# Kernel optimization log

Hardware: AMD Instinct MI355X
Metric: run time of the kernel (lower is better)

Reference implementation:

```python
import jax, jax.numpy as jnp
import numpy as np

NUM_HEADS = 8
SCALE_BASE = 512.0
GN_EPS = 1e-5


def rotate_every_two(x):
    x1 = x[..., ::2]
    x2 = x[..., 1::2]
    return jnp.stack([-x2, x1], axis=-1).reshape(x.shape)


def xpos_apply(x, downscale):
    # x: [B, T, D]; XPOS rotary with length-dependent scale (offset=0)
    L, D = x.shape[1], x.shape[2]
    half = D // 2
    scale_vec = (jnp.arange(0, D, 2, dtype=jnp.float32) + 0.4 * D) / (1.4 * D)  # [half]
    pos = jnp.arange(L, dtype=jnp.float32)
    scale = scale_vec[None, :] ** (pos[:, None] / SCALE_BASE)  # [L, half]
    inv_freq = 1.0 / (10000.0 ** (jnp.arange(half, dtype=jnp.float32) / half))
    sinusoid = pos[:, None] * inv_freq[None, :]  # [L, half]
    sin, cos = jnp.sin(sinusoid), jnp.cos(sinusoid)
    if downscale:
        scale = 1.0 / scale
    sin_s = jnp.repeat(sin * scale, 2, axis=-1)  # duplicate_interleave -> [L, D]
    cos_s = jnp.repeat(cos * scale, 2, axis=-1)
    return x * cos_s + rotate_every_two(x) * sin_s


def decay_mask_fn(T, num_heads):
    # gamma per head; decay stored as log(gamma) so mask = gamma^(i-j) on lower triangle
    s, e = np.log(1.0 / 32.0), np.log(1.0 / 512.0)
    gamma = 1.0 - jnp.exp(jnp.linspace(s, e, num_heads).astype(jnp.float32))
    log_decay = jnp.log(gamma)  # [H], negative
    idx = jnp.arange(T)
    expo = (idx[:, None] - idx[None, :]).astype(jnp.float32)  # i - j
    tri = (idx[:, None] >= idx[None, :])
    expo_safe = jnp.where(tri, expo, 0.0)
    mask = jnp.exp(log_decay[:, None, None] * expo_safe) * tri  # [H, T, T]
    scale = jnp.sqrt(mask.sum(axis=-1, keepdims=True))  # [H, T, 1]
    return mask / scale


def setup_inputs() -> dict:
    key = jax.random.key(0)
    ks = jax.random.split(key, 4)
    B, T, E = 2, 2048, 1024
    V = 2 * E
    return {
        "hidden_states": jax.random.normal(ks[0], (B, T, E), dtype=jnp.float32),
        "w_qkv": jax.random.normal(ks[1], (E, 2 * E + V), dtype=jnp.float32) * 0.02,
        "b_qkv": jnp.zeros((2 * E + V,), dtype=jnp.float32),
        "w_g": jax.random.normal(ks[2], (E, V), dtype=jnp.float32) * 0.02,
        "b_g": jnp.zeros((V,), dtype=jnp.float32),
        "w_p": jax.random.normal(ks[3], (V, E), dtype=jnp.float32) * 0.02,
        "b_p": jnp.zeros((E,), dtype=jnp.float32),
    }


def reference(hidden_states, w_qkv, b_qkv, w_g, b_g, w_p, b_p):
    B, T, E = hidden_states.shape
    H = NUM_HEADS
    V = 2 * E
    dk, dv = E // H, V // H

    qkv = hidden_states @ w_qkv + b_qkv
    q, k, v = qkv[..., :E], qkv[..., E:2 * E], qkv[..., 2 * E:]
    q = xpos_apply(q, downscale=False)
    k = xpos_apply(k, downscale=True)

    # split heads -> [B, H, T, d]
    q = q.reshape(B, T, H, dk).transpose(0, 2, 1, 3)
    k = k.reshape(B, T, H, dk).transpose(0, 2, 1, 3)
    v = v.reshape(B, T, H, dv).transpose(0, 2, 1, 3)

    mask = decay_mask_fn(T, H)  # [H, T, T]

    # parallel retention
    retention = jnp.einsum("bhid,bhjd->bhij", q, k) * (dk ** -0.5)
    retention = retention * mask[None]  # [B, H, T, T]
    out = jnp.einsum("bhij,bhjv->bhiv", retention, v)

    # current_kv = sum_j mask[h, -1, j] * k_j (x) v_j
    curr_kv = jnp.einsum("hj,bhjk,bhjv->bhkv", mask[:, -1, :], k, v)

    retention_out = out.transpose(0, 2, 1, 3).reshape(B, T, V)

    # GroupNorm(num_groups=H, affine=False) over v_dim channels
    g = retention_out.reshape(B * T, H, dv)
    mu = g.mean(axis=-1, keepdims=True)
    var = ((g - mu) ** 2).mean(axis=-1, keepdims=True)
    normed = ((g - mu) / jnp.sqrt(var + GN_EPS)).reshape(B, T, V)

    gated = jax.nn.silu(hidden_states @ w_g + b_g) * normed
    proj = gated @ w_p + b_p
    return proj, curr_kv
```

## Files before the change

kernel.cpp:

```cpp
#include <hip/hip_runtime.h>
#include <math.h>

#define BT      4096
#define T_SEQ   2048
#define E_DIM   1024
#define V_DIM   2048
#define DK      128
#define DV      256
#define QKV_LD  4096

typedef unsigned short ushort_t;
typedef __attribute__((ext_vector_type(8)))  short bf16x8;
typedef __attribute__((ext_vector_type(4)))  unsigned short u16x4;
typedef __attribute__((ext_vector_type(16))) float f32x16;

__device__ __forceinline__ void decay_params(int h, float& ld, float& gamma) {
    const float s0 = -3.4657359027997265f;
    const float e0 = -6.2383246250395092f;
    float lin = s0 + (e0 - s0) * ((float)h * (1.0f / 7.0f));
    gamma = 1.0f - expf(lin);
    ld = logf(gamma);
}

__device__ __forceinline__ short f2bf(float f) {
    unsigned u = __float_as_uint(f);
    unsigned r = (u + 0x7fffu + ((u >> 16) & 1u)) >> 16;
    return (short)r;
}
__device__ __forceinline__ float bf2f(ushort_t u) {
    return __uint_as_float((unsigned)u << 16);
}

__device__ __forceinline__ void async_copy16(void* lds, const void* g) {
    __builtin_amdgcn_global_load_lds(
        (const __attribute__((address_space(1))) unsigned int*)g,
        (__attribute__((address_space(3))) unsigned int*)lds, 16, 0, 0);
}

__global__ __launch_bounds__(256)
void f32_to_bf16_kernel(const float* __restrict__ in, ushort_t* __restrict__ out)
{
    int i = (blockIdx.x * 256 + threadIdx.x) * 8;
    float4 a = *(const float4*)&in[i];
    float4 b = *(const float4*)&in[i + 4];
    bf16x8 o;
    o[0] = f2bf(a.x); o[1] = f2bf(a.y); o[2] = f2bf(a.z); o[3] = f2bf(a.w);
    o[4] = f2bf(b.x); o[5] = f2bf(b.y); o[6] = f2bf(b.z); o[7] = f2bf(b.w);
    *(bf16x8*)&out[i] = o;
}

__global__ __launch_bounds__(256)
void transpose_w_kernel(const float* __restrict__ W, ushort_t* __restrict__ Wt,
                        int K, int N)
{
    __shared__ float tile[32][33];
    const int k0 = blockIdx.y * 32, n0 = blockIdx.x * 32;
    const int t = threadIdx.x;
    const int r = t >> 3, c = (t & 7) * 4;
    float4 v = *(const float4*)&W[(size_t)(k0 + r) * N + n0 + c];
    tile[r][c] = v.x; tile[r][c + 1] = v.y; tile[r][c + 2] = v.z; tile[r][c + 3] = v.w;
    __syncthreads();
    u16x4 o;
    o[0] = (ushort_t)f2bf(tile[c][r]);
    o[1] = (ushort_t)f2bf(tile[c + 1][r]);
    o[2] = (ushort_t)f2bf(tile[c + 2][r]);
    o[3] = (ushort_t)f2bf(tile[c + 3][r]);
    *(u16x4*)&Wt[(size_t)(n0 + r) * K + k0 + c] = o;
}

template<int EPI>
__global__ __launch_bounds__(256)
void gemm_bf16(const ushort_t* __restrict__ A, int lda,
               const ushort_t* __restrict__ Bt, int ldb,
               const float* __restrict__ bias,
               void* __restrict__ Cv, int ldc,
               const void* __restrict__ extra, int lde,
               int nkt)
{
    __shared__ ushort_t As[2 * 128 * 32];
    __shared__ ushort_t Bs[2 * 128 * 32];

    const int tid = threadIdx.x;
    const int w  = tid >> 6, l = tid & 63;
    const int lc = l & 31, q = l >> 5;
    const int wr = w >> 1, wc = w & 1;
    const int m0 = blockIdx.y * 128, n0 = blockIdx.x * 128;

    const int r0 = tid >> 2,         kc0 = (tid & 3) ^ ((r0 >> 1) & 3);
    const int r1 = (256 + tid) >> 2, kc1 = (tid & 3) ^ ((r1 >> 1) & 3);
    const ushort_t* gA0 = A  + (size_t)(m0 + r0) * lda + kc0 * 8;
    const ushort_t* gA1 = A  + (size_t)(m0 + r1) * lda + kc1 * 8;
    const ushort_t* gB0 = Bt + (size_t)(n0 + r0) * ldb + kc0 * 8;
    const ushort_t* gB1 = Bt + (size_t)(n0 + r1) * ldb + kc1 * 8;
    const int s0 = w * 512;
    const int s1 = 2048 + w * 512;

    const int sl = (lc >> 1) & 3;
    int aoff[2][2], boff[2][2];
    #pragma unroll
    for (int mi = 0; mi < 2; ++mi)
        #pragma unroll
        for (int ks = 0; ks < 2; ++ks) {
            const int kc = ks * 2 + q;
            aoff[mi][ks] = ((wr * 64 + mi * 32 + lc) * 4 + (kc ^ sl)) * 8;
            boff[mi][ks] = ((wc * 64 + mi * 32 + lc) * 4 + (kc ^ sl)) * 8;
        }

    f32x16 acc[2][2];
    #pragma unroll
    for (int mi = 0; mi < 2; ++mi)
        #pragma unroll
        for (int ni = 0; ni < 2; ++ni)
            #pragma unroll
            for (int e = 0; e < 16; ++e) acc[mi][ni][e] = 0.0f;

    auto stage = [&](int bb) {
        async_copy16(&As[bb + s0], gA0); async_copy16(&As[bb + s1], gA1);
        async_copy16(&Bs[bb + s0], gB0); async_copy16(&Bs[bb + s1], gB1);
        gA0 += 32; gA1 += 32; gB0 += 32; gB1 += 32;
    };
    auto compute = [&](int cb) {
        bf16x8 a[2][2], b[2][2];
        #pragma unroll
        for (int mi = 0; mi < 2; ++mi)
            #pragma unroll
            for (int ks = 0; ks < 2; ++ks) {
                a[mi][ks] = *(const bf16x8*)&As[cb + aoff[mi][ks]];
                b[mi][ks] = *(const bf16x8*)&Bs[cb + boff[mi][ks]];
            }
        #pragma unroll
        for (int ks = 0; ks < 2; ++ks)
            #pragma unroll
            for (int mi = 0; mi < 2; ++mi)
                #pragma unroll
                for (int ni = 0; ni < 2; ++ni)
                    acc[mi][ni] = __builtin_amdgcn_mfma_f32_32x32x16_bf16(
                        a[mi][ks], b[ni][ks], acc[mi][ni], 0, 0, 0);
    };

    stage(0);
    __syncthreads();
    for (int kt = 0; kt < nkt - 2; kt += 2) {
        stage(4096); compute(0);    __syncthreads();
        stage(0);    compute(4096); __syncthreads();
    }
    stage(4096); compute(0); __syncthreads();
    compute(4096);

    #pragma unroll
    for (int ni = 0; ni < 2; ++ni) {
        const int col = n0 + wc * 64 + ni * 32 + lc;
        const float bb = bias[col];
        #pragma unroll
        for (int mi = 0; mi < 2; ++mi) {
            #pragma unroll
            for (int r = 0; r < 16; ++r) {
                const int row = m0 + wr * 64 + mi * 32 + (r & 3) + 8 * (r >> 2) + 4 * q;
                float val = acc[mi][ni][r] + bb;
                if (EPI == 0) {
                    ((float*)Cv)[(size_t)row * ldc + col] = val;
                } else {
                    const float e = bf2f(((const ushort_t*)extra)[(size_t)row * lde + col]);
                    val = val / (1.0f + expf(-val)) * e;
                    ((ushort_t*)Cv)[(size_t)row * ldc + col] = (ushort_t)f2bf(val);
                }
            }
        }
    }
}

__global__ __launch_bounds__(256)
void gemm_tm64(const ushort_t* __restrict__ A, int lda,
               const ushort_t* __restrict__ Bt, int ldb,
               const float* __restrict__ bias,
               float* __restrict__ C, int ldc, int nkt)
{
    __shared__ ushort_t As[2 * 64 * 32];
    __shared__ ushort_t Bs[2 * 128 * 32];

    const int tid = threadIdx.x;
    const int w  = tid >> 6, l = tid & 63;
    const int lc = l & 31, q = l >> 5;
    const int wr = w >> 1, wc = w & 1;
    const int m0 = blockIdx.y * 64, n0 = blockIdx.x * 128;

    const int rA = tid >> 2,          kcA = (tid & 3) ^ ((rA >> 1) & 3);
    const int rB1 = (256 + tid) >> 2, kcB1 = (tid & 3) ^ ((rB1 >> 1) & 3);
    const ushort_t* gA  = A  + (size_t)(m0 + rA)  * lda + kcA  * 8;
    const ushort_t* gB0 = Bt + (size_t)(n0 + rA)  * ldb + kcA  * 8;
    const ushort_t* gB1 = Bt + (size_t)(n0 + rB1) * ldb + kcB1 * 8;
    const int sA  = w * 512;
    const int sB0 = w * 512;
    const int sB1 = 2048 + w * 512;

    const int sl = (lc >> 1) & 3;
    int aoff[2], boff[2][2];
    #pragma unroll
    for (int ks = 0; ks < 2; ++ks) {
        const int kc = ks * 2 + q;
        const int mrow = wr * 32 + lc;
        aoff[ks] = (mrow * 4 + (kc ^ sl)) * 8;
        #pragma unroll
        for (int ni = 0; ni < 2; ++ni) {
            const int nrow = wc * 64 + ni * 32 + lc;
            boff[ni][ks] = (nrow * 4 + (kc ^ sl)) * 8;
        }
    }

    f32x16 acc[2];
    #pragma unroll
    for (int ni = 0; ni < 2; ++ni)
        #pragma unroll
        for (int e = 0; e < 16; ++e) acc[ni][e] = 0.0f;

    auto stage = [&](int ab, int bb) {
        async_copy16(&As[ab + sA], gA);
        async_copy16(&Bs[bb + sB0], gB0); async_copy16(&Bs[bb + sB1], gB1);
        gA += 32; gB0 += 32; gB1 += 32;
    };
    auto compute = [&](int ab, int bb) {
        bf16x8 a[2], b[2][2];
        #pragma unroll
        for (int ks = 0; ks < 2; ++ks) {
            a[ks] = *(const bf16x8*)&As[ab + aoff[ks]];
            b[0][ks] = *(const bf16x8*)&Bs[bb + boff[0][ks]];
            b[1][ks] = *(const bf16x8*)&Bs[bb + boff[1][ks]];
        }
        #pragma unroll
        for (int ks = 0; ks < 2; ++ks)
            #pragma unroll
            for (int ni = 0; ni < 2; ++ni)
                acc[ni] = __builtin_amdgcn_mfma_f32_32x32x16_bf16(
                    a[ks], b[ni][ks], acc[ni], 0, 0, 0);
    };

    stage(0, 0);
    __syncthreads();
    for (int kt = 0; kt < nkt - 2; kt += 2) {
        stage(2048, 4096); compute(0, 0);       __syncthreads();
        stage(0, 0);       compute(2048, 4096); __syncthreads();
    }
    stage(2048, 4096); compute(0, 0); __syncthreads();
    compute(2048, 4096);

    #pragma unroll
    for (int ni = 0; ni < 2; ++ni) {
        const int col = n0 + wc * 64 + ni * 32 + lc;
        const float bb = bias[col];
        #pragma unroll
        for (int r = 0; r < 16; ++r) {
            const int row = m0 + wr * 32 + (r & 3) + 8 * (r >> 2) + 4 * q;
            C[(size_t)row * ldc + col] = acc[ni][r] + bb;
        }
    }
}

__global__ __launch_bounds__(256)
void qk_prep(const float* __restrict__ qkv,
             ushort_t* __restrict__ qh, ushort_t* __restrict__ kh)
{
    const int row = blockIdx.x;
    const int t = threadIdx.x;
    const int b = row >> 11, trow = row & (T_SEQ - 1);
    const bool isK = t >= 128;
    const int col0 = (t & 127) * 8;
    const int h = col0 >> 7, d = col0 & 127;

    float ld, gamma;
    decay_params(h, ld, gamma);
    const float gsc = expf(isK ? -ld * (float)(trow & 63) : ld * (float)(trow & 63));

    const float* src = qkv + (size_t)row * QKV_LD + (isK ? E_DIM : 0) + col0;
    float4 x0 = *(const float4*)src;
    float4 x1 = *(const float4*)(src + 4);
    float xv[8] = {x0.x, x0.y, x0.z, x0.w, x1.x, x1.y, x1.z, x1.w};

    bf16x8 o;
    #pragma unroll
    for (int pi = 0; pi < 4; ++pi) {
        const int ip = col0 / 2 + pi;
        float sv = (2.0f * (float)ip + 409.6f) * (1.0f / 1433.6f);
        float sc = powf(sv, (float)trow * (1.0f / 512.0f));
        if (isK) sc = 1.0f / sc;
        float invf = powf(10000.0f, -(float)ip * (1.0f / 512.0f));
        float sn, cs;
        sincosf((float)trow * invf, &sn, &cs);
        float c = cs * sc * gsc, s = sn * sc * gsc;
        float a = xv[2 * pi], bb = xv[2 * pi + 1];
        o[2 * pi]     = f2bf(a * c - bb * s);
        o[2 * pi + 1] = f2bf(bb * c + a * s);
    }
    ushort_t* dst = (isK ? kh : qh) + ((size_t)(b * 8 + h) * T_SEQ + trow) * 128 + d;
    *(bf16x8*)dst = o;
}

__global__ __launch_bounds__(256)
void v_transpose(const float* __restrict__ qkv, ushort_t* __restrict__ vt)
{
    __shared__ float tile[32][33];
    const int j0 = blockIdx.x * 32;
    const int zz = blockIdx.y;
    const int bh = zz >> 3, v0 = (zz & 7) * 32;
    const int b = bh >> 3, h = bh & 7;
    const int t = threadIdx.x;
    const int r = t >> 3, c = (t & 7) * 4;

    float4 x = *(const float4*)(qkv + (size_t)(b * T_SEQ + j0 + r) * QKV_LD
                                + 2 * E_DIM + h * DV + v0 + c);
    tile[r][c] = x.x; tile[r][c+1] = x.y; tile[r][c+2] = x.z; tile[r][c+3] = x.w;
    __syncthreads();
    u16x4 o;
    o[0] = (ushort_t)f2bf(tile[c][r]);
    o[1] = (ushort_t)f2bf(tile[c + 1][r]);
    o[2] = (ushort_t)f2bf(tile[c + 2][r]);
    o[3] = (ushort_t)f2bf(tile[c + 3][r]);
    *(u16x4*)&vt[((size_t)bh * 256 + v0 + r) * T_SEQ + j0 + c] = o;
}

__global__ __launch_bounds__(256)
void kt2_kernel(const ushort_t* __restrict__ kh, ushort_t* __restrict__ kt2)
{
    __shared__ ushort_t tile[32][40];
    const int j0 = blockIdx.x * 32;
    const int zz = blockIdx.y;
    const int bh = zz >> 2, k0 = (zz & 3) * 32;
    const int t = threadIdx.x;
    const int r = t >> 3, c = (t & 7) * 4;
    float ld, gamma; decay_params(bh & 7, ld, gamma);
    const float g63 = expf(ld * 63.0f);
    *(u16x4*)&tile[r][c] = *(const u16x4*)&kh[((size_t)bh * T_SEQ + j0 + r) * 128 + k0 + c];
    __syncthreads();
    u16x4 o;
    o[0] = (ushort_t)f2bf(bf2f(tile[c][r])     * g63);
    o[1] = (ushort_t)f2bf(bf2f(tile[c + 1][r]) * g63);
    o[2] = (ushort_t)f2bf(bf2f(tile[c + 2][r]) * g63);
    o[3] = (ushort_t)f2bf(bf2f(tile[c + 3][r]) * g63);
    *(u16x4*)&kt2[((size_t)bh * 128 + k0 + r) * T_SEQ + j0 + c] = o;
}

__global__ __launch_bounds__(256)
void chunk_kv(const ushort_t* __restrict__ vt, const ushort_t* __restrict__ kt2,
              ushort_t* __restrict__ Abuf)
{
    const int c = blockIdx.x;
    const int bh = blockIdx.y;
    const int tid = threadIdx.x;
    const int w = tid >> 6, l = tid & 63, lc = l & 31, q = l >> 5;
    const int j0 = c * 64;

    f32x16 acc[2][4];
    #pragma unroll
    for (int mi = 0; mi < 2; ++mi)
        #pragma unroll
        for (int ni = 0; ni < 4; ++ni)
            #pragma unroll
            for (int e = 0; e < 16; ++e) acc[mi][ni][e] = 0.0f;

    #pragma unroll
    for (int ks = 0; ks < 4; ++ks) {
        bf16x8 a[2], bfr[4];
        #pragma unroll
        for (int mi = 0; mi < 2; ++mi)
            a[mi] = *(const bf16x8*)(vt + ((size_t)bh * 256 + w * 64 + mi * 32 + lc) * T_SEQ
                                     + j0 + ks * 16 + q * 8);
        #pragma unroll
        for (int ni = 0; ni < 4; ++ni)
            bfr[ni] = *(const bf16x8*)(kt2 + ((size_t)bh * 128 + ni * 32 + lc) * T_SEQ
                                       + j0 + ks * 16 + q * 8);
        #pragma unroll
        for (int mi = 0; mi < 2; ++mi)
            #pragma unroll
            for (int ni = 0; ni < 4; ++ni)
                acc[mi][ni] = __builtin_amdgcn_mfma_f32_32x32x16_bf16(
                    a[mi], bfr[ni], acc[mi][ni], 0, 0, 0);
    }

    ushort_t* ab = Abuf + (size_t)(bh * 32 + c) * 256 * 128;
    #pragma unroll
    for (int mi = 0; mi < 2; ++mi)
        #pragma unroll
        for (int ni = 0; ni < 4; ++ni)
            #pragma unroll
            for (int r = 0; r < 16; ++r) {
                const int v = w * 64 + mi * 32 + (r & 3) + 8 * (r >> 2) + 4 * q;
                const int k = ni * 32 + lc;
                ab[(size_t)v * 128 + k] = (ushort_t)f2bf(acc[mi][ni][r]);
            }
}

__global__ __launch_bounds__(256)
void scan_state(const ushort_t* __restrict__ Abuf, ushort_t* __restrict__ St,
                float* __restrict__ ckv)
{
    const int blk = blockIdx.x;
    const int bh = blk >> 7, sub = blk & 127;
    const int tid = threadIdx.x;
    const int v = sub * 2 + (tid >> 7), k = tid & 127;

    float ld, gamma;
    decay_params(bh & 7, ld, gamma);
    const float g64 = expf(ld * 64.0f);

    const size_t base = ((size_t)bh * 32 * 256 + v) * 128 + k;
    const size_t cstr = 256 * 128;
    float s = 0.0f;
    for (int c = 0; c < 32; ++c) {
        const size_t off = base + (size_t)c * cstr;
        St[off] = (ushort_t)f2bf(gamma * s);
        s = g64 * s + bf2f(Abuf[off]);
    }
    const float inv_scale = rsqrtf((1.0f - expf(ld * (float)T_SEQ)) / (1.0f - gamma));
    ckv[((size_t)bh * 128 + k) * 256 + v] = s * inv_scale;
}

__global__ __launch_bounds__(64)
void retention_chunk(const ushort_t* __restrict__ qh,
                     const ushort_t* __restrict__ kh,
                     const ushort_t* __restrict__ vt,
                     const ushort_t* __restrict__ St,
                     ushort_t* __restrict__ normed)
{
    const int it = blockIdx.x;
    const int bh = blockIdx.y;
    const int b = bh >> 3, h = bh & 7;
    const int c = it >> 1, w = it & 1;
    const int l = threadIdx.x, lc = l & 31, q = l >> 5;
    const int i0 = it * 32;
    const size_t bhT = (size_t)bh * T_SEQ;

    float ld, gamma;
    decay_params(h, ld, gamma);

    bf16x8 qf[8];
    {
        const ushort_t* qp = qh + (bhT + i0 + lc) * 128 + q * 8;
        #pragma unroll
        for (int c8 = 0; c8 < 8; ++c8)
            qf[c8] = *(const bf16x8*)(qp + c8 * 16);
    }

    f32x16 acc[8];
    #pragma unroll
    for (int vg = 0; vg < 8; ++vg)
        #pragma unroll
        for (int e = 0; e < 16; ++e) acc[vg][e] = 0.0f;

    if (c > 0) {
        const ushort_t* sp = St + ((size_t)(bh * 32 + c) * 256 + lc) * 128 + q * 8;
        #pragma unroll
        for (int vg = 0; vg < 8; ++vg) {
            const ushort_t* spv = sp + (size_t)vg * 32 * 128;
            #pragma unroll
            for (int ks = 0; ks < 8; ++ks) {
                bf16x8 sb = *(const bf16x8*)(spv + ks * 16);
                acc[vg] = __builtin_amdgcn_mfma_f32_32x32x16_bf16(
                    qf[ks], sb, acc[vg], 0, 0, 0);
            }
        }
    }

    for (int jt2 = 0; jt2 <= w; ++jt2) {
        const int j0 = c * 64 + jt2 * 32;

        f32x16 s;
        #pragma unroll
        for (int e = 0; e < 16; ++e) s[e] = 0.0f;
        const ushort_t* kp = kh + (bhT + j0 + lc) * 128 + q * 8;
        #pragma unroll
        for (int c8 = 0; c8 < 8; ++c8) {
            bf16x8 ka = *(const bf16x8*)(kp + c8 * 16);
            s = __builtin_amdgcn_mfma_f32_32x32x16_bf16(ka, qf[c8], s, 0, 0, 0);
        }

        float sv[16];
        #pragma unroll
        for (int r = 0; r < 16; ++r) {
            float val = s[r];
            if (jt2 == w) {
                int jr_ = (r & 3) + 8 * (r >> 2) + 4 * q;
                val = (jr_ <= lc) ? val : 0.0f;
            }
            sv[r] = val;
        }

        bf16x8 pa0, pa1;
        #pragma unroll
        for (int e = 0; e < 4; ++e) {
            float t1 = __shfl_xor(sv[e + 4], 32);
            float t0 = __shfl_xor(sv[e], 32);
            pa0[e]     = f2bf(q ? t1 : sv[e]);
            pa0[e + 4] = f2bf(q ? sv[e + 4] : t0);
            float t3 = __shfl_xor(sv[e + 12], 32);
            float t2 = __shfl_xor(sv[e + 8], 32);
            pa1[e]     = f2bf(q ? t3 : sv[e + 8]);
            pa1[e + 4] = f2bf(q ? sv[e + 12] : t2);
        }

        #pragma unroll
        for (int vg = 0; vg < 8; ++vg) {
            const ushort_t* vp = vt + ((size_t)bh * 256 + vg * 32 + lc) * T_SEQ + j0 + q * 8;
            bf16x8 vb0 = *(const bf16x8*)vp;
            bf16x8 vb1 = *(const bf16x8*)(vp + 16);
            acc[vg] = __builtin_amdgcn_mfma_f32_32x32x16_bf16(pa0, vb0, acc[vg], 0, 0, 0);
            acc[vg] = __builtin_amdgcn_mfma_f32_32x32x16_bf16(pa1, vb1, acc[vg], 0, 0, 0);
        }
    }

    #pragma unroll
    for (int r = 0; r < 16; ++r) {
        const int il = (r & 3) + 8 * (r >> 2) + 4 * q;
        const int i  = i0 + il;
        float denom = (1.0f - expf(ld * (float)(i + 1))) / (1.0f - gamma);
        float fs = 0.08838834764831845f * rsqrtf(denom);
        float vals[8];
        float a1 = 0.0f, a2 = 0.0f;
        #pragma unroll
        for (int vg = 0; vg < 8; ++vg) {
            float x = acc[vg][r] * fs;
            vals[vg] = x;
            a1 += x; a2 += x * x;
        }
        a1 += __shfl_xor(a1, 1);  a2 += __shfl_xor(a2, 1);
        a1 += __shfl_xor(a1, 2);  a2 += __shfl_xor(a2, 2);
        a1 += __shfl_xor(a1, 4);  a2 += __shfl_xor(a2, 4);
        a1 += __shfl_xor(a1, 8);  a2 += __shfl_xor(a2, 8);
        a1 += __shfl_xor(a1, 16); a2 += __shfl_xor(a2, 16);
        float mu = a1 * (1.0f / 256.0f);
        float var = a2 * (1.0f / 256.0f) - mu * mu;
        float rs = rsqrtf(var + 1e-5f);
        ushort_t* op = normed + ((size_t)(b * T_SEQ + i)) * V_DIM + h * DV + lc;
        #pragma unroll
        for (int vg = 0; vg < 8; ++vg)
            op[vg * 32] = (ushort_t)f2bf((vals[vg] - mu) * rs);
    }
}

extern "C" void kernel_launch(void* const* d_in, const int* in_sizes, int n_in,
                              void* d_out, int out_size, void* d_ws, size_t ws_size,
                              hipStream_t stream)
{
    const float* hs    = (const float*)d_in[0];
    const float* w_qkv = (const float*)d_in[1];
    const float* b_qkv = (const float*)d_in[2];
    const float* w_g   = (const float*)d_in[3];
    const float* b_g   = (const float*)d_in[4];
    const float* w_p   = (const float*)d_in[5];
    const float* b_p   = (const float*)d_in[6];
    float* out = (float*)d_out;

    const size_t MB = 1024 * 1024;
    float*    qkv      = (float*)d_ws;
    ushort_t* Abuf     = (ushort_t*)d_ws;
    ushort_t* normed   = (ushort_t*)d_ws;
    ushort_t* Stbuf    = (ushort_t*)((char*)d_ws + 32 * MB);
    ushort_t* gated_bf = (ushort_t*)((char*)d_ws + 32 * MB);
    ushort_t* wg_t     = (ushort_t*)((char*)d_ws + 56 * MB);
    ushort_t* wp_t     = (ushort_t*)((char*)d_ws + 60 * MB);
    ushort_t* qh       = (ushort_t*)((char*)d_ws + 64 * MB);
    ushort_t* vt       = (ushort_t*)((char*)d_ws + 72 * MB);
    ushort_t* wqkv_t   = (ushort_t*)((char*)d_ws + 88 * MB);
    ushort_t* kh       = (ushort_t*)((char*)d_ws + 88 * MB);
    ushort_t* hs_bf    = (ushort_t*)d_out;
    ushort_t* kt2      = (ushort_t*)((char*)d_out + 8 * MB);
    float*    ckv_out  = out + (size_t)BT * E_DIM;

    f32_to_bf16_kernel<<<dim3(2048), 256, 0, stream>>>(hs, hs_bf);
    transpose_w_kernel<<<dim3(128, 32), 256, 0, stream>>>(w_qkv, wqkv_t, E_DIM, 4096);

    gemm_bf16<0><<<dim3(32, 32), 256, 0, stream>>>(
        hs_bf, E_DIM, wqkv_t, E_DIM, b_qkv, qkv, QKV_LD, nullptr, 0, E_DIM / 32);

    qk_prep<<<dim3(BT), 256, 0, stream>>>(qkv, qh, kh);
    v_transpose<<<dim3(64, 128), 256, 0, stream>>>(qkv, vt);
    kt2_kernel<<<dim3(64, 64), 256, 0, stream>>>(kh, kt2);

    chunk_kv<<<dim3(32, 16), 256, 0, stream>>>(vt, kt2, Abuf);
    scan_state<<<dim3(2048), 256, 0, stream>>>(Abuf, Stbuf, ckv_out);
    retention_chunk<<<dim3(64, 16), 64, 0, stream>>>(qh, kh, vt, Stbuf, normed);

    transpose_w_kernel<<<dim3(64, 32), 256, 0, stream>>>(w_g, wg_t, E_DIM, V_DIM);
    transpose_w_kernel<<<dim3(32, 64), 256, 0, stream>>>(w_p, wp_t, V_DIM, E_DIM);

    gemm_bf16<1><<<dim3(16, 32), 256, 0, stream>>>(
        hs_bf, E_DIM, wg_t, E_DIM, b_g, gated_bf, V_DIM, normed, V_DIM, E_DIM / 32);

    gemm_tm64<<<dim3(8, 64), 256, 0, stream>>>(
        gated_bf, V_DIM, wp_t, V_DIM, b_p, out, E_DIM, V_DIM / 32);
}
```

Measured before the change: 339.8 us.

## Triple-buffer GEMM LDS tiles with vmcnt-based waits and use fast math in qk_prep

```diff
diff --git a/kernel.cpp b/kernel.cpp
--- a/kernel.cpp
+++ b/kernel.cpp
@@ -77,8 +77,8 @@
                const void* __restrict__ extra, int lde,
                int nkt)
 {
-    __shared__ ushort_t As[2 * 128 * 32];
-    __shared__ ushort_t Bs[2 * 128 * 32];
+    __shared__ ushort_t As[3 * 128 * 32];
+    __shared__ ushort_t Bs[3 * 128 * 32];
 
     const int tid = threadIdx.x;
     const int w  = tid >> 6, l = tid & 63;
@@ -138,14 +138,24 @@
                         a[mi][ks], b[ni][ks], acc[mi][ni], 0, 0, 0);
     };
 
-    stage(0);
-    __syncthreads();
-    for (int kt = 0; kt < nkt - 2; kt += 2) {
-        stage(4096); compute(0);    __syncthreads();
-        stage(0);    compute(4096); __syncthreads();
-    }
-    stage(4096); compute(0); __syncthreads();
-    compute(4096);
+    stage(0); stage(4096);
+    int bs = 8192;
+    int bc = 0;
+    for (int kt = 0; kt < nkt - 2; ++kt) {
+        asm volatile("s_waitcnt vmcnt(4)" ::: "memory");
+        __builtin_amdgcn_s_barrier();
+        stage(bs);
+        compute(bc);
+        bs = bc;
+        bc = (bc == 8192) ? 0 : bc + 4096;
+    }
+    asm volatile("s_waitcnt vmcnt(4)" ::: "memory");
+    __builtin_amdgcn_s_barrier();
+    compute(bc);
+    bc = (bc == 8192) ? 0 : bc + 4096;
+    asm volatile("s_waitcnt vmcnt(0)" ::: "memory");
+    __builtin_amdgcn_s_barrier();
+    compute(bc);
 
     #pragma unroll
     for (int ni = 0; ni < 2; ++ni) {
@@ -175,8 +185,8 @@
                const float* __restrict__ bias,
                float* __restrict__ C, int ldc, int nkt)
 {
-    __shared__ ushort_t As[2 * 64 * 32];
-    __shared__ ushort_t Bs[2 * 128 * 32];
+    __shared__ ushort_t As[3 * 64 * 32];
+    __shared__ ushort_t Bs[3 * 128 * 32];
 
     const int tid = threadIdx.x;
     const int w  = tid >> 6, l = tid & 63;
@@ -234,14 +244,26 @@
                     a[ks], b[ni][ks], acc[ni], 0, 0, 0);
     };
 
-    stage(0, 0);
-    __syncthreads();
-    for (int kt = 0; kt < nkt - 2; kt += 2) {
-        stage(2048, 4096); compute(0, 0);       __syncthreads();
-        stage(0, 0);       compute(2048, 4096); __syncthreads();
-    }
-    stage(2048, 4096); compute(0, 0); __syncthreads();
-    compute(2048, 4096);
+    stage(0, 0); stage(2048, 4096);
+    int as_ = 4096, bs_ = 8192;
+    int ac_ = 0,    bc_ = 0;
+    for (int kt = 0; kt < nkt - 2; ++kt) {
+        asm volatile("s_waitcnt vmcnt(3)" ::: "memory");
+        __builtin_amdgcn_s_barrier();
+        stage(as_, bs_);
+        compute(ac_, bc_);
+        as_ = ac_; bs_ = bc_;
+        ac_ = (ac_ == 4096) ? 0 : ac_ + 2048;
+        bc_ = (bc_ == 8192) ? 0 : bc_ + 4096;
+    }
+    asm volatile("s_waitcnt vmcnt(3)" ::: "memory");
+    __builtin_amdgcn_s_barrier();
+    compute(ac_, bc_);
+    ac_ = (ac_ == 4096) ? 0 : ac_ + 2048;
+    bc_ = (bc_ == 8192) ? 0 : bc_ + 4096;
+    asm volatile("s_waitcnt vmcnt(0)" ::: "memory");
+    __builtin_amdgcn_s_barrier();
+    compute(ac_, bc_);
 
     #pragma unroll
     for (int ni = 0; ni < 2; ++ni) {
@@ -268,21 +290,23 @@
 
     float ld, gamma;
     decay_params(h, ld, gamma);
-    const float gsc = expf(isK ? -ld * (float)(trow & 63) : ld * (float)(trow & 63));
+    const float gsc = __expf(isK ? -ld * (float)(trow & 63) : ld * (float)(trow & 63));
 
     const float* src = qkv + (size_t)row * QKV_LD + (isK ? E_DIM : 0) + col0;
     float4 x0 = *(const float4*)src;
     float4 x1 = *(const float4*)(src + 4);
     float xv[8] = {x0.x, x0.y, x0.z, x0.w, x1.x, x1.y, x1.z, x1.w};
 
+    const float tf = (float)trow * (1.0f / 512.0f);
     bf16x8 o;
     #pragma unroll
     for (int pi = 0; pi < 4; ++pi) {
         const int ip = col0 / 2 + pi;
         float sv = (2.0f * (float)ip + 409.6f) * (1.0f / 1433.6f);
-        float sc = powf(sv, (float)trow * (1.0f / 512.0f));
-        if (isK) sc = 1.0f / sc;
-        float invf = powf(10000.0f, -(float)ip * (1.0f / 512.0f));
+        float e = __logf(sv) * tf;
+        if (isK) e = -e;
+        float sc = __expf(e);
+        float invf = __expf((float)ip * -0.017988946038999563f);
         float sn, cs;
         sincosf((float)trow * invf, &sn, &cs);
         float c = cs * sc * gsc, s = sn * sc * gsc;
```

New measurement: 307.7 us. -9.4%, faster.
